# Kernel tuning notes

Measured on AMD Instinct MI355X. Metric: run time of the kernel, lower is better.

The kernel has to match this reference:

```python
import jax, jax.numpy as jnp
import numpy as np

B, S_PREV, E, H, LOW = 8, 4095, 2048, 16, 512
HD = E // H  # 128
ROPE_BASE = 10000.0


def _rope(x, pos):
    # x: [..., S, d], pos: [S]; half-split rotary
    d = x.shape[-1]
    half = d // 2
    inv_freq = 1.0 / (ROPE_BASE ** (jnp.arange(half, dtype=jnp.float32) / half))
    ang = pos.astype(jnp.float32)[:, None] * inv_freq  # [S, half]
    cos, sin = jnp.cos(ang), jnp.sin(ang)
    x1, x2 = x[..., :half], x[..., half:]
    return jnp.concatenate([x1 * cos - x2 * sin, x1 * sin + x2 * cos], axis=-1)


def setup_inputs() -> dict:
    key = jax.random.key(0)
    ks = jax.random.split(key, 10)

    def w(k, *shape):
        return jax.random.normal(k, shape, dtype=jnp.float32) * (1.0 / np.float32(np.sqrt(shape[0])))

    return {
        "x": jax.random.normal(ks[0], (B, 1, E), dtype=jnp.float32),
        "ckv_cache": jax.random.normal(ks[1], (B, S_PREV, LOW), dtype=jnp.float32),
        "kr_cache": jax.random.normal(ks[2], (B, S_PREV, HD), dtype=jnp.float32),
        "Wdq": w(ks[3], E, E),
        "Wuq": w(ks[4], E, E),
        "Wqr": w(ks[5], E, HD),
        "Wdkv": w(ks[6], E, LOW),
        "Wkr": w(ks[7], E, HD),
        "fused_upsample": w(ks[8], LOW, 2 * E),
        "Wo": w(ks[9], E, E),
    }


def reference(x, ckv_cache, kr_cache, Wdq, Wuq, Wqr, Wdkv, Wkr, fused_upsample, Wo):
    Bx = x.shape[0]
    # update compressed KV caches with the current token
    ckv = jnp.concatenate([ckv_cache, x @ Wdkv], axis=1)            # [B,S,LOW]
    kr = jnp.concatenate([kr_cache, x @ Wkr], axis=1)               # [B,S,HD]
    S = ckv.shape[1]
    up = ckv @ fused_upsample                                       # [B,S,2E]
    k_up, v = up[..., :E], up[..., E:]
    Kc = k_up.reshape(Bx, S, H, HD).transpose(0, 2, 1, 3)           # [B,H,S,HD]
    Kr = _rope(kr, jnp.arange(S))                                   # [B,S,HD] shared rope-K
    Kr = jnp.broadcast_to(Kr[:, None], (Bx, H, S, HD))
    v = v.reshape(Bx, S, H, HD).transpose(0, 2, 1, 3)               # [B,H,S,HD]
    # query path
    Cq = x @ Wdq                                                    # [B,1,E]
    Qc = (Cq @ Wuq).reshape(Bx, 1, H, HD).transpose(0, 2, 1, 3)     # [B,H,1,HD]
    Qr = _rope(Cq @ Wqr, jnp.arange(S - 1, S))                      # [B,1,HD] at last pos
    Qr = jnp.broadcast_to(Qr[:, None], (Bx, H, 1, HD))
    q = jnp.concatenate([Qc, Qr], axis=-1)                          # [B,H,1,2HD]
    k = jnp.concatenate([Kc, Kr], axis=-1)                          # [B,H,S,2HD]
    scores = jnp.einsum('bhqd,bhkd->bhqk', q, k) / np.float32(np.sqrt(2 * HD))
    attn = jax.nn.softmax(scores, axis=-1)
    o = jnp.einsum('bhqk,bhkd->bhqd', attn, v)                      # [B,H,1,HD]
    out = o.transpose(0, 2, 1, 3).reshape(Bx, 1, E) @ Wo            # [B,1,E]
    return out
```

## Files before the change

### kernel.cpp

```cpp
#include <hip/hip_runtime.h>
#include <hip/hip_bf16.h>

#define B_ 8
#define SPREV 4095
#define S_ 4096
#define E_ 2048
#define H_ 16
#define HD_ 128
#define LOW_ 512
#define NCH 64
#define CHK 64

typedef short s8v __attribute__((ext_vector_type(8)));
typedef float f4v __attribute__((ext_vector_type(4)));

__device__ __forceinline__ short f2bf_s(float f) {
  return (short)__bfloat16_as_ushort(__float2bfloat16(f));
}
__device__ __forceinline__ float bf2f(unsigned short h) {
  union { unsigned u; float f; } v; v.u = ((unsigned)h) << 16;
  return v.f;
}

__global__ __launch_bounds__(256) void init_kernel(float* __restrict__ ws_pre,
                                                   float* __restrict__ out,
                                                   float2* __restrict__ tab2) {
  int i = blockIdx.x * 256 + threadIdx.x;
  if (i < 55296) ws_pre[i] = 0.f;
  else if (i < 71680) out[i - 55296] = 0.f;
  int s = i >> 6, j = i & 63;
  float invf = powf(10000.0f, -(float)j * (1.0f / 64.0f));
  float sn, cs; sincosf((float)s * invf, &sn, &cs);
  tab2[i] = make_float2(cs, sn);
}

__global__ __launch_bounds__(128) void matvec8(
    const float* __restrict__ x, int K,
    const float* __restrict__ W0, int N0, float* __restrict__ o0,
    const float* __restrict__ W1, int N1, float* __restrict__ o1,
    const float* __restrict__ W2, int N2, float* __restrict__ o2)
{
  int cb = blockIdx.x;
  int nb0 = N0 >> 7, nb1 = N1 >> 7;
  const float* W; float* o; int N, colbase;
  if (cb < nb0)            { W = W0; o = o0; N = N0; colbase = cb << 7; }
  else if (cb < nb0 + nb1) { W = W1; o = o1; N = N1; colbase = (cb - nb0) << 7; }
  else                     { W = W2; o = o2; N = N2; colbase = (cb - nb0 - nb1) << 7; }
  int col = colbase + threadIdx.x;
  int k0 = blockIdx.y * 32;
  float acc[B_];
  #pragma unroll
  for (int b = 0; b < B_; ++b) acc[b] = 0.f;
  const float* Wp = W + (size_t)k0 * N + col;
  #pragma unroll 8
  for (int k = 0; k < 32; ++k) {
    float wv = Wp[(size_t)k * N];
    #pragma unroll
    for (int b = 0; b < B_; ++b)
      acc[b] = fmaf(x[b * K + k0 + k], wv, acc[b]);
  }
  #pragma unroll
  for (int b = 0; b < B_; ++b) atomicAdd(&o[b * N + col], acc[b]);
}

__global__ __launch_bounds__(256) void qeff_kernel(
    const float* __restrict__ Qc, const float* __restrict__ FU,
    unsigned short* __restrict__ qeff)
{
  int bx = blockIdx.x, b = blockIdx.y, t = threadIdx.x;
  int h = bx >> 2, lq = bx & 3;
  int g = t >> 4, li = t & 15;
  __shared__ float qs[HD_];
  if (t < 128) qs[t] = Qc[b * E_ + h * HD_ + t];
  __syncthreads();
  f4v q0 = *(const f4v*)&qs[li * 8];
  f4v q1 = *(const f4v*)&qs[li * 8 + 4];
  #pragma unroll 2
  for (int p = 0; p < 8; ++p) {
    int l = lq * 128 + p * 16 + g;
    const f4v* w4 = (const f4v*)(FU + (size_t)l * (2 * E_) + h * HD_ + li * 8);
    f4v w0 = w4[0], w1 = w4[1];
    float a = w0[0]*q0[0] + w0[1]*q0[1] + w0[2]*q0[2] + w0[3]*q0[3]
            + w1[0]*q1[0] + w1[1]*q1[1] + w1[2]*q1[2] + w1[3]*q1[3];
    a += __shfl_xor(a, 1); a += __shfl_xor(a, 2);
    a += __shfl_xor(a, 4); a += __shfl_xor(a, 8);
    if (li == 0) qeff[(size_t)(b * H_ + h) * LOW_ + l] = (unsigned short)f2bf_s(a);
  }
}

__global__ __launch_bounds__(256) void attn_kernel(
    const float* __restrict__ ckv_cache, const float* __restrict__ ckv_new,
    const unsigned short* __restrict__ qeff,
    const float* __restrict__ kr_cache, const float* __restrict__ kr_new,
    const float* __restrict__ qr_pre, const float2* __restrict__ tab2,
    unsigned short* __restrict__ acc_part, float* __restrict__ m_part,
    float* __restrict__ l_part)
{
  int chunk = blockIdx.x, b = blockIdx.y;
  int tid = threadIdx.x;
  int w = tid >> 6, lane = tid & 63;
  int kg = lane >> 4, l16 = lane & 15;
  __shared__ float S_lds[16 * 64];
  __shared__ unsigned short P_lds[16 * 64];
  __shared__ float qr_sh[128];
  __shared__ float rope_lds[64];

  if (tid < 64) {
    float invf = powf(10000.0f, -(float)tid * (1.0f / 64.0f));
    float x1 = qr_pre[b * HD_ + tid], x2 = qr_pre[b * HD_ + 64 + tid];
    float sn, cs; sincosf(4095.0f * invf, &sn, &cs);
    qr_sh[tid]      = x1 * cs - x2 * sn;
    qr_sh[64 + tid] = x1 * sn + x2 * cs;
  }
  __syncthreads();

  {
    int s_loc = w * 16 + l16;
    int s = chunk * CHK + s_loc;
    const float* crow = (s == S_ - 1) ? (ckv_new + b * LOW_)
                                      : (ckv_cache + ((size_t)b * SPREV + s) * LOW_);
    f4v acc = {0.f, 0.f, 0.f, 0.f};
    const s8v* qf = (const s8v*)(qeff + (size_t)(b * H_ + l16) * LOW_);
    #pragma unroll
    for (int kt = 0; kt < 16; ++kt) {
      s8v a = qf[kt * 4 + kg];
      const float* cp = crow + kt * 32 + kg * 8;
      f4v c0 = *(const f4v*)cp;
      f4v c1 = *(const f4v*)(cp + 4);
      s8v bv;
      bv[0]=f2bf_s(c0[0]); bv[1]=f2bf_s(c0[1]); bv[2]=f2bf_s(c0[2]); bv[3]=f2bf_s(c0[3]);
      bv[4]=f2bf_s(c1[0]); bv[5]=f2bf_s(c1[1]); bv[6]=f2bf_s(c1[2]); bv[7]=f2bf_s(c1[3]);
      acc = __builtin_amdgcn_mfma_f32_16x16x32_bf16(a, bv, acc, 0, 0, 0);
    }
    #pragma unroll
    for (int r = 0; r < 4; ++r) {
      int h = kg * 4 + r;
      S_lds[h * 64 + (s_loc ^ ((h & 7) << 2))] = acc[r];
    }
    const float* krp = (s == S_ - 1) ? (kr_new + b * HD_)
                                     : (kr_cache + ((size_t)b * SPREV + s) * HD_);
    float rdot = 0.f;
    #pragma unroll
    for (int q = 0; q < 4; ++q) {
      int j = kg * 16 + q * 4;
      f4v x1 = *(const f4v*)&krp[j];
      f4v x2 = *(const f4v*)&krp[64 + j];
      f4v qa = *(const f4v*)&qr_sh[j];
      f4v qb = *(const f4v*)&qr_sh[64 + j];
      const float2* tp = &tab2[(size_t)s * 64 + j];
      #pragma unroll
      for (int k = 0; k < 4; ++k) {
        float2 cs2 = tp[k];
        rdot += qa[k] * (x1[k] * cs2.x - x2[k] * cs2.y)
              + qb[k] * (x1[k] * cs2.y + x2[k] * cs2.x);
      }
    }
    rdot += __shfl_xor(rdot, 16);
    rdot += __shfl_xor(rdot, 32);
    if (kg == 0) rope_lds[s_loc] = rdot;
  }
  __syncthreads();

  if (w == 0) {
    int h = l16, part = kg;
    float v[16];
    #pragma unroll
    for (int jj = 0; jj < 4; ++jj) {
      int sb = part * 16 + jj * 4;
      f4v sv = *(const f4v*)&S_lds[h * 64 + (sb ^ ((h & 7) << 2))];
      f4v rv = *(const f4v*)&rope_lds[sb];
      #pragma unroll
      for (int q = 0; q < 4; ++q) v[jj * 4 + q] = (sv[q] + rv[q]) * 0.0625f;
    }
    float m = v[0];
    #pragma unroll
    for (int j = 1; j < 16; ++j) m = fmaxf(m, v[j]);
    m = fmaxf(m, __shfl_xor(m, 16));
    m = fmaxf(m, __shfl_xor(m, 32));
    float lsum = 0.f;
    #pragma unroll
    for (int j = 0; j < 16; ++j) { v[j] = expf(v[j] - m); lsum += v[j]; }
    lsum += __shfl_xor(lsum, 16);
    lsum += __shfl_xor(lsum, 32);
    #pragma unroll
    for (int jj = 0; jj < 8; ++jj) {
      int sb = part * 16 + jj * 2;
      unsigned pk = (unsigned)(unsigned short)f2bf_s(v[jj*2]) |
                    ((unsigned)(unsigned short)f2bf_s(v[jj*2+1]) << 16);
      *(unsigned*)&P_lds[h * 64 + (sb ^ ((h & 7) << 3))] = pk;
    }
    if (part == 0) {
      int idx = (b * NCH + chunk) * H_ + h;
      m_part[idx] = m;
      l_part[idx] = lsum;
    }
  }
  __syncthreads();

  {
    s8v pa[2];
    const float* rp[2][8];
    #pragma unroll
    for (int kt = 0; kt < 2; ++kt) {
      int so = kt * 32 + kg * 8;
      pa[kt] = *(const s8v*)&P_lds[l16 * 64 + (so ^ ((l16 & 7) << 3))];
      #pragma unroll
      for (int i = 0; i < 8; ++i) {
        int s = chunk * CHK + so + i;
        rp[kt][i] = (s == S_ - 1) ? (ckv_new + b * LOW_)
                                  : (ckv_cache + ((size_t)b * SPREV + s) * LOW_);
      }
    }
    f4v oa[8];
    #pragma unroll
    for (int nt = 0; nt < 8; ++nt) oa[nt] = {0.f, 0.f, 0.f, 0.f};
    #pragma unroll
    for (int nt = 0; nt < 8; ++nt) {
      int l = w * 128 + nt * 16 + l16;
      #pragma unroll
      for (int kt = 0; kt < 2; ++kt) {
        s8v bv;
        #pragma unroll
        for (int i = 0; i < 8; ++i) bv[i] = (short)f2bf_s(rp[kt][i][l]);
        oa[nt] = __builtin_amdgcn_mfma_f32_16x16x32_bf16(pa[kt], bv, oa[nt], 0, 0, 0);
      }
    }
    size_t base = (size_t)(b * NCH + chunk) * H_;
    #pragma unroll
    for (int nt = 0; nt < 8; ++nt) {
      int l = w * 128 + nt * 16 + l16;
      #pragma unroll
      for (int r = 0; r < 4; ++r) {
        int h = kg * 4 + r;
        acc_part[(base + h) * LOW_ + l] = (unsigned short)f2bf_s(oa[nt][r]);
      }
    }
  }
}

__global__ __launch_bounds__(128) void reduce_proj_kernel(
    const float* __restrict__ m_part, const float* __restrict__ l_part,
    const unsigned short* __restrict__ acc_part, const float* __restrict__ FU,
    float* __restrict__ o_heads)
{
  int h = blockIdx.x, b = blockIdx.y, lz = blockIdx.z, t = threadIdx.x;
  __shared__ float wls[NCH];
  __shared__ float Linv_s;
  __shared__ float pa0[128], pa1[128];
  __shared__ float wl_sh[64];
  if (t < 64) {
    float mc = m_part[(b * NCH + t) * H_ + h];
    float M = mc;
    #pragma unroll
    for (int d = 1; d < 64; d <<= 1) M = fmaxf(M, __shfl_xor(M, d));
    float wc = expf(mc - M);
    float L = l_part[(b * NCH + t) * H_ + h] * wc;
    #pragma unroll
    for (int d = 1; d < 64; d <<= 1) L += __shfl_xor(L, d);
    wls[t] = wc;
    if (t == 0) Linv_s = 1.0f / L;
  }
  __syncthreads();
  {
    int p = t & 31, ch = t >> 5;
    int l0 = lz * 64 + p * 2;
    float a0 = 0.f, a1 = 0.f;
    const unsigned short* ap =
        acc_part + ((size_t)(b * NCH + ch * 16) * H_ + h) * LOW_ + l0;
    #pragma unroll 4
    for (int c = 0; c < 16; ++c) {
      unsigned pk = *(const unsigned*)(ap + (size_t)c * H_ * LOW_);
      float wc = wls[ch * 16 + c];
      a0 = fmaf(bf2f((unsigned short)(pk & 0xffffu)), wc, a0);
      a1 = fmaf(bf2f((unsigned short)(pk >> 16)),     wc, a1);
    }
    pa0[t] = a0; pa1[t] = a1;
  }
  __syncthreads();
  if (t < 32) {
    float inv = Linv_s;
    float s0 = pa0[t] + pa0[t + 32] + pa0[t + 64] + pa0[t + 96];
    float s1 = pa1[t] + pa1[t + 32] + pa1[t + 64] + pa1[t + 96];
    wl_sh[t * 2]     = s0 * inv;
    wl_sh[t * 2 + 1] = s1 * inv;
  }
  __syncthreads();
  {
    float a = 0.f;
    const float* fp = FU + (size_t)(lz * 64) * (2 * E_) + E_ + h * HD_ + t;
    #pragma unroll 4
    for (int l = 0; l < 64; ++l)
      a = fmaf(wl_sh[l], fp[(size_t)l * (2 * E_)], a);
    atomicAdd(&o_heads[(b * H_ + h) * HD_ + t], a);
  }
}

extern "C" void kernel_launch(void* const* d_in, const int* in_sizes, int n_in,
                              void* d_out, int out_size, void* d_ws, size_t ws_size,
                              hipStream_t stream)
{
  const float* x    = (const float*)d_in[0];
  const float* ckvc = (const float*)d_in[1];
  const float* krc  = (const float*)d_in[2];
  const float* Wdq  = (const float*)d_in[3];
  const float* Wuq  = (const float*)d_in[4];
  const float* Wqr  = (const float*)d_in[5];
  const float* Wdkv = (const float*)d_in[6];
  const float* Wkr  = (const float*)d_in[7];
  const float* FU   = (const float*)d_in[8];
  const float* Wo   = (const float*)d_in[9];
  float* out = (float*)d_out;

  char* ws = (char*)d_ws;
  float* Cq             = (float*)(ws + 0);
  float* Qc             = (float*)(ws + 65536);
  float* qr_pre         = (float*)(ws + 131072);
  float* ckvn           = (float*)(ws + 135168);
  float* krn            = (float*)(ws + 151552);
  float* o_heads        = (float*)(ws + 155648);
  unsigned short* qeff  = (unsigned short*)(ws + 221184);
  float* m_part         = (float*)(ws + 352256);
  float* l_part         = (float*)(ws + 385024);
  unsigned short* accp  = (unsigned short*)(ws + 417792);
  float2* tab2          = (float2*)(ws + 8806400);

  init_kernel<<<1024, 256, 0, stream>>>((float*)ws, out, tab2);

  matvec8<<<dim3(21, 64), 128, 0, stream>>>(x, E_, Wdq, E_, Cq,
                                            Wdkv, LOW_, ckvn, Wkr, HD_, krn);
  matvec8<<<dim3(17, 64), 128, 0, stream>>>(Cq, E_, Wuq, E_, Qc,
                                            Wqr, HD_, qr_pre,
                                            (const float*)nullptr, 0, (float*)nullptr);
  qeff_kernel<<<dim3(64, 8), 256, 0, stream>>>(Qc, FU, qeff);
  attn_kernel<<<dim3(64, 8), 256, 0, stream>>>(ckvc, ckvn, qeff, krc, krn,
                                               qr_pre, tab2, accp, m_part, l_part);
  reduce_proj_kernel<<<dim3(16, 8, 8), 128, 0, stream>>>(m_part, l_part, accp,
                                                         FU, o_heads);
  matvec8<<<dim3(16, 64), 128, 0, stream>>>(o_heads, E_, Wo, E_, out,
                                            (const float*)nullptr, 0, (float*)nullptr,
                                            (const float*)nullptr, 0, (float*)nullptr);
}
```

Measured before the change: 83.98 us.

## Split rope score computation into separate kernel and dual-accumulate MFMA chain

Moves the rotary-key score dot product out of the attention kernel into a new rope_kernel that writes per-position rope scores to workspace, which the attention kernel then reads during softmax. The attention kernel also splits its MFMA accumulation across two accumulators to shorten the dependency chain. This is meant to cut register pressure and latency in the attention kernel, at the cost of an extra launch and a global round trip for the rope scores.

```diff
diff --git a/kernel.cpp b/kernel.cpp
--- a/kernel.cpp
+++ b/kernel.cpp
@@ -88,11 +88,49 @@
   }
 }
 
+__global__ __launch_bounds__(256) void rope_kernel(
+    const float* __restrict__ kr_cache, const float* __restrict__ kr_new,
+    const float* __restrict__ qr_pre, const float2* __restrict__ tab2,
+    float* __restrict__ score_r)
+{
+  int bx = blockIdx.x, b = blockIdx.y, t = threadIdx.x;
+  int g = t >> 4, li = t & 15;
+  int s_base = bx * 256;
+  __shared__ float qr[128];
+  if (t < 64) {
+    float invf = powf(10000.0f, -(float)t * (1.0f / 64.0f));
+    float x1 = qr_pre[b * HD_ + t], x2 = qr_pre[b * HD_ + 64 + t];
+    float sn, cs; sincosf(4095.0f * invf, &sn, &cs);
+    qr[t]      = x1 * cs - x2 * sn;
+    qr[64 + t] = x1 * sn + x2 * cs;
+  }
+  __syncthreads();
+  f4v qa = *(const f4v*)&qr[li * 4];
+  f4v qb = *(const f4v*)&qr[64 + li * 4];
+  #pragma unroll 2
+  for (int p = 0; p < 16; ++p) {
+    int s = s_base + p * 16 + g;
+    const float* krp = (s == S_ - 1) ? (kr_new + b * HD_)
+                                     : (kr_cache + ((size_t)b * SPREV + s) * HD_);
+    f4v x1 = *(const f4v*)&krp[li * 4];
+    f4v x2 = *(const f4v*)&krp[64 + li * 4];
+    const float2* tp = &tab2[(size_t)s * 64 + li * 4];
+    float dot = 0.f;
+    #pragma unroll
+    for (int q = 0; q < 4; ++q) {
+      float2 cs2 = tp[q];
+      dot += qa[q] * (x1[q] * cs2.x - x2[q] * cs2.y)
+           + qb[q] * (x1[q] * cs2.y + x2[q] * cs2.x);
+    }
+    dot += __shfl_xor(dot, 1); dot += __shfl_xor(dot, 2);
+    dot += __shfl_xor(dot, 4); dot += __shfl_xor(dot, 8);
+    if (li == 0) score_r[b * S_ + s] = dot;
+  }
+}
+
 __global__ __launch_bounds__(256) void attn_kernel(
     const float* __restrict__ ckv_cache, const float* __restrict__ ckv_new,
-    const unsigned short* __restrict__ qeff,
-    const float* __restrict__ kr_cache, const float* __restrict__ kr_new,
-    const float* __restrict__ qr_pre, const float2* __restrict__ tab2,
+    const unsigned short* __restrict__ qeff, const float* __restrict__ score_r,
     unsigned short* __restrict__ acc_part, float* __restrict__ m_part,
     float* __restrict__ l_part)
 {
@@ -102,62 +140,38 @@
   int kg = lane >> 4, l16 = lane & 15;
   __shared__ float S_lds[16 * 64];
   __shared__ unsigned short P_lds[16 * 64];
-  __shared__ float qr_sh[128];
-  __shared__ float rope_lds[64];
-
-  if (tid < 64) {
-    float invf = powf(10000.0f, -(float)tid * (1.0f / 64.0f));
-    float x1 = qr_pre[b * HD_ + tid], x2 = qr_pre[b * HD_ + 64 + tid];
-    float sn, cs; sincosf(4095.0f * invf, &sn, &cs);
-    qr_sh[tid]      = x1 * cs - x2 * sn;
-    qr_sh[64 + tid] = x1 * sn + x2 * cs;
-  }
-  __syncthreads();
 
   {
     int s_loc = w * 16 + l16;
     int s = chunk * CHK + s_loc;
     const float* crow = (s == S_ - 1) ? (ckv_new + b * LOW_)
                                       : (ckv_cache + ((size_t)b * SPREV + s) * LOW_);
-    f4v acc = {0.f, 0.f, 0.f, 0.f};
+    f4v acc0 = {0.f, 0.f, 0.f, 0.f};
+    f4v acc1 = {0.f, 0.f, 0.f, 0.f};
     const s8v* qf = (const s8v*)(qeff + (size_t)(b * H_ + l16) * LOW_);
     #pragma unroll
-    for (int kt = 0; kt < 16; ++kt) {
-      s8v a = qf[kt * 4 + kg];
-      const float* cp = crow + kt * 32 + kg * 8;
-      f4v c0 = *(const f4v*)cp;
-      f4v c1 = *(const f4v*)(cp + 4);
-      s8v bv;
-      bv[0]=f2bf_s(c0[0]); bv[1]=f2bf_s(c0[1]); bv[2]=f2bf_s(c0[2]); bv[3]=f2bf_s(c0[3]);
-      bv[4]=f2bf_s(c1[0]); bv[5]=f2bf_s(c1[1]); bv[6]=f2bf_s(c1[2]); bv[7]=f2bf_s(c1[3]);
-      acc = __builtin_amdgcn_mfma_f32_16x16x32_bf16(a, bv, acc, 0, 0, 0);
+    for (int kt = 0; kt < 8; ++kt) {
+      #pragma unroll
+      for (int half = 0; half < 2; ++half) {
+        int kk = kt * 2 + half;
+        s8v a = qf[kk * 4 + kg];
+        const float* cp = crow + kk * 32 + kg * 8;
+        f4v c0 = *(const f4v*)cp;
+        f4v c1 = *(const f4v*)(cp + 4);
+        s8v bv;
+        bv[0]=f2bf_s(c0[0]); bv[1]=f2bf_s(c0[1]); bv[2]=f2bf_s(c0[2]); bv[3]=f2bf_s(c0[3]);
+        bv[4]=f2bf_s(c1[0]); bv[5]=f2bf_s(c1[1]); bv[6]=f2bf_s(c1[2]); bv[7]=f2bf_s(c1[3]);
+        if (half == 0)
+          acc0 = __builtin_amdgcn_mfma_f32_16x16x32_bf16(a, bv, acc0, 0, 0, 0);
+        else
+          acc1 = __builtin_amdgcn_mfma_f32_16x16x32_bf16(a, bv, acc1, 0, 0, 0);
+      }
     }
     #pragma unroll
     for (int r = 0; r < 4; ++r) {
       int h = kg * 4 + r;
-      S_lds[h * 64 + (s_loc ^ ((h & 7) << 2))] = acc[r];
-    }
-    const float* krp = (s == S_ - 1) ? (kr_new + b * HD_)
-                                     : (kr_cache + ((size_t)b * SPREV + s) * HD_);
-    float rdot = 0.f;
-    #pragma unroll
-    for (int q = 0; q < 4; ++q) {
-      int j = kg * 16 + q * 4;
-      f4v x1 = *(const f4v*)&krp[j];
-      f4v x2 = *(const f4v*)&krp[64 + j];
-      f4v qa = *(const f4v*)&qr_sh[j];
-      f4v qb = *(const f4v*)&qr_sh[64 + j];
-      const float2* tp = &tab2[(size_t)s * 64 + j];
-      #pragma unroll
-      for (int k = 0; k < 4; ++k) {
-        float2 cs2 = tp[k];
-        rdot += qa[k] * (x1[k] * cs2.x - x2[k] * cs2.y)
-              + qb[k] * (x1[k] * cs2.y + x2[k] * cs2.x);
-      }
-    }
-    rdot += __shfl_xor(rdot, 16);
-    rdot += __shfl_xor(rdot, 32);
-    if (kg == 0) rope_lds[s_loc] = rdot;
+      S_lds[h * 64 + (s_loc ^ ((h & 7) << 2))] = acc0[r] + acc1[r];
+    }
   }
   __syncthreads();
 
@@ -168,7 +182,7 @@
     for (int jj = 0; jj < 4; ++jj) {
       int sb = part * 16 + jj * 4;
       f4v sv = *(const f4v*)&S_lds[h * 64 + (sb ^ ((h & 7) << 2))];
-      f4v rv = *(const f4v*)&rope_lds[sb];
+      f4v rv = *(const f4v*)&score_r[b * S_ + chunk * CHK + sb];
       #pragma unroll
       for (int q = 0; q < 4; ++q) v[jj * 4 + q] = (sv[q] + rv[q]) * 0.0625f;
     }
@@ -321,8 +335,9 @@
   unsigned short* qeff  = (unsigned short*)(ws + 221184);
   float* m_part         = (float*)(ws + 352256);
   float* l_part         = (float*)(ws + 385024);
-  unsigned short* accp  = (unsigned short*)(ws + 417792);
-  float2* tab2          = (float2*)(ws + 8806400);
+  float* score_r        = (float*)(ws + 417792);
+  unsigned short* accp  = (unsigned short*)(ws + 548864);
+  float2* tab2          = (float2*)(ws + 8937472);
 
   init_kernel<<<1024, 256, 0, stream>>>((float*)ws, out, tab2);
 
@@ -332,8 +347,9 @@
                                             Wqr, HD_, qr_pre,
                                             (const float*)nullptr, 0, (float*)nullptr);
   qeff_kernel<<<dim3(64, 8), 256, 0, stream>>>(Qc, FU, qeff);
-  attn_kernel<<<dim3(64, 8), 256, 0, stream>>>(ckvc, ckvn, qeff, krc, krn,
-                                               qr_pre, tab2, accp, m_part, l_part);
+  rope_kernel<<<dim3(16, 8), 256, 0, stream>>>(krc, krn, qr_pre, tab2, score_r);
+  attn_kernel<<<dim3(64, 8), 256, 0, stream>>>(ckvc, ckvn, qeff, score_r,
+                                               accp, m_part, l_part);
   reduce_proj_kernel<<<dim3(16, 8, 8), 128, 0, stream>>>(m_part, l_part, accp,
                                                          FU, o_heads);
   matvec8<<<dim3(16, 64), 128, 0, stream>>>(o_heads, E_, Wo, E_, out,
```

Measured after the change: 89.83 us. 1.07x slower.

## Double attention block width, compute rope trig inline, parallelize softmax across waves

Applied to the files above, without the earlier changes.

The attention kernel moves from 256 to 512 threads per block. The score MFMA's K dimension is split across two wave groups, and their partial results are summed from two LDS buffers. Softmax is now spread over all 8 waves, each handling two heads, instead of running on a single wave. The precomputed cos/sin table is dropped and rope angles are computed inline with exp2f/sincosf, which removes 2MB of table writes in init and the table reads in attention at the cost of more transcendental math per element.

```diff
diff --git a/kernel.cpp b/kernel.cpp
--- a/kernel.cpp
+++ b/kernel.cpp
@@ -10,6 +10,7 @@
 #define LOW_ 512
 #define NCH 64
 #define CHK 64
+#define L2INV 0.207620506f
 
 typedef short s8v __attribute__((ext_vector_type(8)));
 typedef float f4v __attribute__((ext_vector_type(4)));
@@ -23,15 +24,10 @@
 }
 
 __global__ __launch_bounds__(256) void init_kernel(float* __restrict__ ws_pre,
-                                                   float* __restrict__ out,
-                                                   float2* __restrict__ tab2) {
+                                                   float* __restrict__ out) {
   int i = blockIdx.x * 256 + threadIdx.x;
   if (i < 55296) ws_pre[i] = 0.f;
   else if (i < 71680) out[i - 55296] = 0.f;
-  int s = i >> 6, j = i & 63;
-  float invf = powf(10000.0f, -(float)j * (1.0f / 64.0f));
-  float sn, cs; sincosf((float)s * invf, &sn, &cs);
-  tab2[i] = make_float2(cs, sn);
 }
 
 __global__ __launch_bounds__(128) void matvec8(
@@ -88,11 +84,11 @@
   }
 }
 
-__global__ __launch_bounds__(256) void attn_kernel(
+__global__ __launch_bounds__(512) void attn_kernel(
     const float* __restrict__ ckv_cache, const float* __restrict__ ckv_new,
     const unsigned short* __restrict__ qeff,
     const float* __restrict__ kr_cache, const float* __restrict__ kr_new,
-    const float* __restrict__ qr_pre, const float2* __restrict__ tab2,
+    const float* __restrict__ qr_pre,
     unsigned short* __restrict__ acc_part, float* __restrict__ m_part,
     float* __restrict__ l_part)
 {
@@ -100,13 +96,13 @@
   int tid = threadIdx.x;
   int w = tid >> 6, lane = tid & 63;
   int kg = lane >> 4, l16 = lane & 15;
-  __shared__ float S_lds[16 * 64];
+  __shared__ float S_lds[2][16 * 64];
   __shared__ unsigned short P_lds[16 * 64];
   __shared__ float qr_sh[128];
   __shared__ float rope_lds[64];
 
   if (tid < 64) {
-    float invf = powf(10000.0f, -(float)tid * (1.0f / 64.0f));
+    float invf = exp2f(-L2INV * (float)tid);
     float x1 = qr_pre[b * HD_ + tid], x2 = qr_pre[b * HD_ + 64 + tid];
     float sn, cs; sincosf(4095.0f * invf, &sn, &cs);
     qr_sh[tid]      = x1 * cs - x2 * sn;
@@ -115,81 +111,87 @@
   __syncthreads();
 
   {
-    int s_loc = w * 16 + l16;
+    int kh = w >> 2;
+    int s_loc = (w & 3) * 16 + l16;
     int s = chunk * CHK + s_loc;
     const float* crow = (s == S_ - 1) ? (ckv_new + b * LOW_)
                                       : (ckv_cache + ((size_t)b * SPREV + s) * LOW_);
-    f4v acc = {0.f, 0.f, 0.f, 0.f};
+    f4v acc0 = {0.f, 0.f, 0.f, 0.f};
+    f4v acc1 = {0.f, 0.f, 0.f, 0.f};
     const s8v* qf = (const s8v*)(qeff + (size_t)(b * H_ + l16) * LOW_);
     #pragma unroll
-    for (int kt = 0; kt < 16; ++kt) {
-      s8v a = qf[kt * 4 + kg];
-      const float* cp = crow + kt * 32 + kg * 8;
-      f4v c0 = *(const f4v*)cp;
-      f4v c1 = *(const f4v*)(cp + 4);
-      s8v bv;
-      bv[0]=f2bf_s(c0[0]); bv[1]=f2bf_s(c0[1]); bv[2]=f2bf_s(c0[2]); bv[3]=f2bf_s(c0[3]);
-      bv[4]=f2bf_s(c1[0]); bv[5]=f2bf_s(c1[1]); bv[6]=f2bf_s(c1[2]); bv[7]=f2bf_s(c1[3]);
-      acc = __builtin_amdgcn_mfma_f32_16x16x32_bf16(a, bv, acc, 0, 0, 0);
+    for (int kt = 0; kt < 4; ++kt) {
+      #pragma unroll
+      for (int half = 0; half < 2; ++half) {
+        int kk = kh * 8 + kt * 2 + half;
+        s8v a = qf[kk * 4 + kg];
+        const float* cp = crow + kk * 32 + kg * 8;
+        f4v c0 = *(const f4v*)cp;
+        f4v c1 = *(const f4v*)(cp + 4);
+        s8v bv;
+        bv[0]=f2bf_s(c0[0]); bv[1]=f2bf_s(c0[1]); bv[2]=f2bf_s(c0[2]); bv[3]=f2bf_s(c0[3]);
+        bv[4]=f2bf_s(c1[0]); bv[5]=f2bf_s(c1[1]); bv[6]=f2bf_s(c1[2]); bv[7]=f2bf_s(c1[3]);
+        if (half == 0)
+          acc0 = __builtin_amdgcn_mfma_f32_16x16x32_bf16(a, bv, acc0, 0, 0, 0);
+        else
+          acc1 = __builtin_amdgcn_mfma_f32_16x16x32_bf16(a, bv, acc1, 0, 0, 0);
+      }
     }
     #pragma unroll
     for (int r = 0; r < 4; ++r) {
       int h = kg * 4 + r;
-      S_lds[h * 64 + (s_loc ^ ((h & 7) << 2))] = acc[r];
-    }
-    const float* krp = (s == S_ - 1) ? (kr_new + b * HD_)
-                                     : (kr_cache + ((size_t)b * SPREV + s) * HD_);
-    float rdot = 0.f;
-    #pragma unroll
-    for (int q = 0; q < 4; ++q) {
-      int j = kg * 16 + q * 4;
-      f4v x1 = *(const f4v*)&krp[j];
-      f4v x2 = *(const f4v*)&krp[64 + j];
-      f4v qa = *(const f4v*)&qr_sh[j];
-      f4v qb = *(const f4v*)&qr_sh[64 + j];
-      const float2* tp = &tab2[(size_t)s * 64 + j];
-      #pragma unroll
-      for (int k = 0; k < 4; ++k) {
-        float2 cs2 = tp[k];
-        rdot += qa[k] * (x1[k] * cs2.x - x2[k] * cs2.y)
-              + qb[k] * (x1[k] * cs2.y + x2[k] * cs2.x);
-      }
-    }
-    rdot += __shfl_xor(rdot, 16);
-    rdot += __shfl_xor(rdot, 32);
-    if (kg == 0) rope_lds[s_loc] = rdot;
-  }
-  __syncthreads();
-
-  if (w == 0) {
-    int h = l16, part = kg;
-    float v[16];
-    #pragma unroll
-    for (int jj = 0; jj < 4; ++jj) {
-      int sb = part * 16 + jj * 4;
-      f4v sv = *(const f4v*)&S_lds[h * 64 + (sb ^ ((h & 7) << 2))];
-      f4v rv = *(const f4v*)&rope_lds[sb];
-      #pragma unroll
-      for (int q = 0; q < 4; ++q) v[jj * 4 + q] = (sv[q] + rv[q]) * 0.0625f;
-    }
-    float m = v[0];
-    #pragma unroll
-    for (int j = 1; j < 16; ++j) m = fmaxf(m, v[j]);
+      S_lds[kh][h * 64 + (s_loc ^ ((h & 7) << 2))] = acc0[r] + acc1[r];
+    }
+    if (w < 4) {
+      const float* krp = (s == S_ - 1) ? (kr_new + b * HD_)
+                                       : (kr_cache + ((size_t)b * SPREV + s) * HD_);
+      float fs = (float)s;
+      float rdot = 0.f;
+      #pragma unroll
+      for (int q = 0; q < 4; ++q) {
+        int j = kg * 16 + q * 4;
+        f4v x1 = *(const f4v*)&krp[j];
+        f4v x2 = *(const f4v*)&krp[64 + j];
+        f4v qa = *(const f4v*)&qr_sh[j];
+        f4v qb = *(const f4v*)&qr_sh[64 + j];
+        #pragma unroll
+        for (int k2 = 0; k2 < 4; ++k2) {
+          float invf = exp2f(-L2INV * (float)(j + k2));
+          float sn, cs; sincosf(fs * invf, &sn, &cs);
+          rdot += qa[k2] * (x1[k2] * cs - x2[k2] * sn)
+                + qb[k2] * (x1[k2] * sn + x2[k2] * cs);
+        }
+      }
+      rdot += __shfl_xor(rdot, 16);
+      rdot += __shfl_xor(rdot, 32);
+      if (kg == 0) rope_lds[s_loc] = rdot;
+    }
+  }
+  __syncthreads();
+
+  {
+    int half = lane >> 5;
+    int h = w * 2 + half;
+    int sl = lane & 31;
+    int s0 = sl * 2;
+    int c2 = (h & 7) << 2;
+    float v0 = (S_lds[0][h * 64 + (s0 ^ c2)] + S_lds[1][h * 64 + (s0 ^ c2)]
+                + rope_lds[s0]) * 0.0625f;
+    float v1 = (S_lds[0][h * 64 + ((s0 + 1) ^ c2)] + S_lds[1][h * 64 + ((s0 + 1) ^ c2)]
+                + rope_lds[s0 + 1]) * 0.0625f;
+    float m = fmaxf(v0, v1);
+    m = fmaxf(m, __shfl_xor(m, 1));  m = fmaxf(m, __shfl_xor(m, 2));
+    m = fmaxf(m, __shfl_xor(m, 4));  m = fmaxf(m, __shfl_xor(m, 8));
     m = fmaxf(m, __shfl_xor(m, 16));
-    m = fmaxf(m, __shfl_xor(m, 32));
-    float lsum = 0.f;
-    #pragma unroll
-    for (int j = 0; j < 16; ++j) { v[j] = expf(v[j] - m); lsum += v[j]; }
+    float e0 = expf(v0 - m), e1 = expf(v1 - m);
+    float lsum = e0 + e1;
+    lsum += __shfl_xor(lsum, 1);  lsum += __shfl_xor(lsum, 2);
+    lsum += __shfl_xor(lsum, 4);  lsum += __shfl_xor(lsum, 8);
     lsum += __shfl_xor(lsum, 16);
-    lsum += __shfl_xor(lsum, 32);
-    #pragma unroll
-    for (int jj = 0; jj < 8; ++jj) {
-      int sb = part * 16 + jj * 2;
-      unsigned pk = (unsigned)(unsigned short)f2bf_s(v[jj*2]) |
-                    ((unsigned)(unsigned short)f2bf_s(v[jj*2+1]) << 16);
-      *(unsigned*)&P_lds[h * 64 + (sb ^ ((h & 7) << 3))] = pk;
-    }
-    if (part == 0) {
+    unsigned pk = (unsigned)(unsigned short)f2bf_s(e0) |
+                  ((unsigned)(unsigned short)f2bf_s(e1) << 16);
+    *(unsigned*)&P_lds[h * 64 + (s0 ^ ((h & 7) << 3))] = pk;
+    if (sl == 0) {
       int idx = (b * NCH + chunk) * H_ + h;
       m_part[idx] = m;
       l_part[idx] = lsum;
@@ -211,12 +213,12 @@
                                   : (ckv_cache + ((size_t)b * SPREV + s) * LOW_);
       }
     }
-    f4v oa[8];
-    #pragma unroll
-    for (int nt = 0; nt < 8; ++nt) oa[nt] = {0.f, 0.f, 0.f, 0.f};
-    #pragma unroll
-    for (int nt = 0; nt < 8; ++nt) {
-      int l = w * 128 + nt * 16 + l16;
+    f4v oa[4];
+    #pragma unroll
+    for (int nt = 0; nt < 4; ++nt) oa[nt] = {0.f, 0.f, 0.f, 0.f};
+    #pragma unroll
+    for (int nt = 0; nt < 4; ++nt) {
+      int l = w * 64 + nt * 16 + l16;
       #pragma unroll
       for (int kt = 0; kt < 2; ++kt) {
         s8v bv;
@@ -227,8 +229,8 @@
     }
     size_t base = (size_t)(b * NCH + chunk) * H_;
     #pragma unroll
-    for (int nt = 0; nt < 8; ++nt) {
-      int l = w * 128 + nt * 16 + l16;
+    for (int nt = 0; nt < 4; ++nt) {
+      int l = w * 64 + nt * 16 + l16;
       #pragma unroll
       for (int r = 0; r < 4; ++r) {
         int h = kg * 4 + r;
@@ -322,9 +324,8 @@
   float* m_part         = (float*)(ws + 352256);
   float* l_part         = (float*)(ws + 385024);
   unsigned short* accp  = (unsigned short*)(ws + 417792);
-  float2* tab2          = (float2*)(ws + 8806400);
-
-  init_kernel<<<1024, 256, 0, stream>>>((float*)ws, out, tab2);
+
+  init_kernel<<<280, 256, 0, stream>>>((float*)ws, out);
 
   matvec8<<<dim3(21, 64), 128, 0, stream>>>(x, E_, Wdq, E_, Cq,
                                             Wdkv, LOW_, ckvn, Wkr, HD_, krn);
@@ -332,8 +333,8 @@
                                             Wqr, HD_, qr_pre,
                                             (const float*)nullptr, 0, (float*)nullptr);
   qeff_kernel<<<dim3(64, 8), 256, 0, stream>>>(Qc, FU, qeff);
-  attn_kernel<<<dim3(64, 8), 256, 0, stream>>>(ckvc, ckvn, qeff, krc, krn,
-                                               qr_pre, tab2, accp, m_part, l_part);
+  attn_kernel<<<dim3(64, 8), 512, 0, stream>>>(ckvc, ckvn, qeff, krc, krn,
+                                               qr_pre, accp, m_part, l_part);
   reduce_proj_kernel<<<dim3(16, 8, 8), 128, 0, stream>>>(m_part, l_part, accp,
                                                          FU, o_heads);
   matvec8<<<dim3(16, 64), 128, 0, stream>>>(o_heads, E_, Wo, E_, out,
```

Result: no change. 83.11 us (-1.0%).
